# Kernel optimization log

Measured on AMD Instinct MI355X. Metric: run time of the kernel, lower is better.

The kernel has to match this reference:

```python
import jax, jax.numpy as jnp
from jax import lax
import numpy as np

N, C_IN, C_OUT, H, W_SP = 16, 16, 64, 256, 256
K, STRIDE, PAD = 3, 1, 1


def setup_inputs() -> dict:
    key = jax.random.key(0)
    k1, k2 = jax.random.split(key)
    x = jax.random.normal(k1, (N, C_IN, H, W_SP), dtype=jnp.float32)
    # One 3x3 filter per output channel (C_out independent Super0Net branches),
    # stacked into a single OIHW weight -> equivalent to the concatenated loop.
    W = jax.random.normal(k2, (C_OUT, C_IN, K, K), dtype=jnp.float32) * 0.05
    return {"x": x, "W": W}


def reference(x, W):
    # Fused form of: for ch in range(C_out): conv_ch(x) ; concat(dim=1).
    # Each branch is a Conv2d(C_in, 1, 3, stride=1, padding=1, bias=False).
    return lax.conv_general_dilated(
        x, W,
        window_strides=(STRIDE, STRIDE),
        padding=((PAD, PAD), (PAD, PAD)),
        dimension_numbers=("NCHW", "OIHW", "NCHW"),
    )
```

## Files before the change

### kernel.cpp

```cpp
#include <hip/hip_runtime.h>
#include <hip/hip_bf16.h>

typedef __attribute__((ext_vector_type(8))) __bf16 bf16x8;
typedef __attribute__((ext_vector_type(4))) float f32x4;

constexpr int CI_ = 16, CO_ = 64, H_ = 256, W_ = 256;
constexpr int WTROW = 168;
constexpr int RSZ = 258 * 32;

__device__ __forceinline__ unsigned swz(unsigned o) {
  return o ^ (((o >> 7) & 7u) << 4);
}

__global__ void transform_x_kernel(const float* __restrict__ x,
                                   unsigned short* __restrict__ xt) {
  int t = blockIdx.x * 256 + threadIdx.x;
  int p0 = t << 2;
  int w = p0 & 255;
  int h = (p0 >> 8) & 255;
  int n = p0 >> 16;
  const float* src = x + ((size_t)n * CI_) * (H_ * W_) + h * W_ + w;
  unsigned short tmp[64];
#pragma unroll
  for (int ci = 0; ci < 16; ++ci) {
    float4 v = *(const float4*)(src + (size_t)ci * (H_ * W_));
    tmp[0 * 16 + ci] = __builtin_bit_cast(unsigned short, (__bf16)v.x);
    tmp[1 * 16 + ci] = __builtin_bit_cast(unsigned short, (__bf16)v.y);
    tmp[2 * 16 + ci] = __builtin_bit_cast(unsigned short, (__bf16)v.z);
    tmp[3 * 16 + ci] = __builtin_bit_cast(unsigned short, (__bf16)v.w);
  }
  uint4* dst = (uint4*)(xt + (size_t)p0 * 16);
#pragma unroll
  for (int q = 0; q < 8; ++q) dst[q] = ((const uint4*)tmp)[q];
}

__global__ void transform_w_kernel(const float* __restrict__ Wg,
                                   unsigned short* __restrict__ wt) {
  int idx = blockIdx.x * 256 + threadIdx.x;
  int co = idx / WTROW;
  int kk = idx - co * WTROW;
  float v = 0.f;
  if (kk < 144) {
    int t = kk >> 4;
    int ci = kk & 15;
    v = Wg[(co * 16 + ci) * 9 + t];
  }
  wt[idx] = __builtin_bit_cast(unsigned short, (__bf16)v);
}

__global__ __launch_bounds__(256) void conv_mfma_kernel(
    const unsigned short* __restrict__ xt, const unsigned short* __restrict__ wt,
    float* __restrict__ out) {
  __shared__ unsigned char xs[3 * RSZ];
  __shared__ unsigned short wlds[CO_][WTROW];

  int tid = threadIdx.x;
  int bid = blockIdx.x;
  int h = bid & 255;
  int n = bid >> 8;

  {
    const uint4* src = (const uint4*)wt;
    uint4* dst = (uint4*)&wlds[0][0];
    for (int c = tid; c < 1344; c += 256) dst[c] = src[c];
  }
  {
    const uint4* srcbase = (const uint4*)xt;
    for (int c = tid; c < 1536; c += 256) {
      int r = c >> 9;
      int j = c & 511;
      int hh = h - 1 + r;
      uint4 v = make_uint4(0u, 0u, 0u, 0u);
      if (hh >= 0 && hh < 256)
        v = srcbase[(size_t)(n * 256 + hh) * 512 + j];
      *(uint4*)(xs + r * RSZ + swz(32u + 16u * (unsigned)j)) = v;
    }
    if (tid < 12) {
      int r = tid >> 2;
      int q = tid & 3;
      unsigned off = ((q >> 1) ? 257u * 32u : 0u) + (q & 1) * 16u;
      *(uint4*)(xs + r * RSZ + swz(off)) = make_uint4(0u, 0u, 0u, 0u);
    }
  }
  __syncthreads();

  int lane = tid & 63;
  int wave = tid >> 6;
  int col = lane & 15;
  int g = lane >> 4;

  f32x4 acc[4][4];
#pragma unroll
  for (int i = 0; i < 4; ++i)
#pragma unroll
    for (int j = 0; j < 4; ++j) acc[i][j] = (f32x4){0.f, 0.f, 0.f, 0.f};

  int pxb = wave * 64 + 4 * col;

#pragma unroll
  for (int s = 0; s < 5; ++s) {
    bf16x8 a[4];
#pragma unroll
    for (int cb = 0; cb < 4; ++cb)
      a[cb] = *(const bf16x8*)&wlds[cb * 16 + col][s * 32 + 8 * g];

    int tap = 2 * s + (g >> 1);
    if (tap > 8) tap = 8;
    int kh = tap / 3;
    int kw = tap - kh * 3;
    int ci0 = (g & 1) * 8;

    bf16x8 b[4];
#pragma unroll
    for (int pb = 0; pb < 4; ++pb) {
      unsigned wp = (unsigned)(pxb + pb + kw);
      b[pb] = *(const bf16x8*)(xs + kh * RSZ + swz(wp * 32u + ci0 * 2u));
    }

#pragma unroll
    for (int cb = 0; cb < 4; ++cb)
#pragma unroll
      for (int pb = 0; pb < 4; ++pb)
        acc[cb][pb] = __builtin_amdgcn_mfma_f32_16x16x32_bf16(
            a[cb], b[pb], acc[cb][pb], 0, 0, 0);
  }

  size_t obase = ((size_t)n * CO_ * H_ + h) * W_ + pxb;
#pragma unroll
  for (int cb = 0; cb < 4; ++cb) {
#pragma unroll
    for (int r = 0; r < 4; ++r) {
      int co = cb * 16 + g * 4 + r;
      f32x4 v = {acc[cb][0][r], acc[cb][1][r], acc[cb][2][r], acc[cb][3][r]};
      *(f32x4*)(out + obase + (size_t)co * (H_ * W_)) = v;
    }
  }
}

extern "C" void kernel_launch(void* const* d_in, const int* in_sizes, int n_in,
                              void* d_out, int out_size, void* d_ws, size_t ws_size,
                              hipStream_t stream) {
  const float* x = (const float*)d_in[0];
  const float* W = (const float*)d_in[1];
  float* out = (float*)d_out;

  unsigned short* xt = (unsigned short*)d_ws;
  unsigned short* wt = xt + (size_t)16 * 256 * 256 * 16;

  transform_x_kernel<<<1024, 256, 0, stream>>>(x, xt);
  transform_w_kernel<<<42, 256, 0, stream>>>(W, wt);
  conv_mfma_kernel<<<4096, 256, 0, stream>>>(xt, wt, out);
}
```

Baseline: 343.5 us.

## Fuse input NCHW-to-NHWC bf16 transform into conv kernel's LDS load

Removes the separate input transform kernel and its workspace round-trip. The conv kernel now reads fp32 NCHW rows directly, converts them to bf16 and writes channel-interleaved pairs into the swizzled LDS tile. The block index is also remapped so that neighbouring blocks land on different XCDs. The risk is redundant global reads, since each input row is fetched by three blocks in fp32, and narrower 4-byte LDS stores.

```diff
diff --git a/kernel.cpp b/kernel.cpp
--- a/kernel.cpp
+++ b/kernel.cpp
@@ -10,28 +10,6 @@
 
 __device__ __forceinline__ unsigned swz(unsigned o) {
   return o ^ (((o >> 7) & 7u) << 4);
-}
-
-__global__ void transform_x_kernel(const float* __restrict__ x,
-                                   unsigned short* __restrict__ xt) {
-  int t = blockIdx.x * 256 + threadIdx.x;
-  int p0 = t << 2;
-  int w = p0 & 255;
-  int h = (p0 >> 8) & 255;
-  int n = p0 >> 16;
-  const float* src = x + ((size_t)n * CI_) * (H_ * W_) + h * W_ + w;
-  unsigned short tmp[64];
-#pragma unroll
-  for (int ci = 0; ci < 16; ++ci) {
-    float4 v = *(const float4*)(src + (size_t)ci * (H_ * W_));
-    tmp[0 * 16 + ci] = __builtin_bit_cast(unsigned short, (__bf16)v.x);
-    tmp[1 * 16 + ci] = __builtin_bit_cast(unsigned short, (__bf16)v.y);
-    tmp[2 * 16 + ci] = __builtin_bit_cast(unsigned short, (__bf16)v.z);
-    tmp[3 * 16 + ci] = __builtin_bit_cast(unsigned short, (__bf16)v.w);
-  }
-  uint4* dst = (uint4*)(xt + (size_t)p0 * 16);
-#pragma unroll
-  for (int q = 0; q < 8; ++q) dst[q] = ((const uint4*)tmp)[q];
 }
 
 __global__ void transform_w_kernel(const float* __restrict__ Wg,
@@ -48,32 +26,52 @@
   wt[idx] = __builtin_bit_cast(unsigned short, (__bf16)v);
 }
 
-__global__ __launch_bounds__(256) void conv_mfma_kernel(
-    const unsigned short* __restrict__ xt, const unsigned short* __restrict__ wt,
+__global__ __launch_bounds__(256) void conv_fused_kernel(
+    const float* __restrict__ x, const unsigned short* __restrict__ wt,
     float* __restrict__ out) {
   __shared__ unsigned char xs[3 * RSZ];
   __shared__ unsigned short wlds[CO_][WTROW];
 
   int tid = threadIdx.x;
   int bid = blockIdx.x;
-  int h = bid & 255;
-  int n = bid >> 8;
+  int linear = (bid & 7) * 512 + (bid >> 3);
+  int h = linear & 255;
+  int n = linear >> 8;
+
+  int lane = tid & 63;
+  int wave = tid >> 6;
 
   {
     const uint4* src = (const uint4*)wt;
     uint4* dst = (uint4*)&wlds[0][0];
     for (int c = tid; c < 1344; c += 256) dst[c] = src[c];
   }
+
   {
-    const uint4* srcbase = (const uint4*)xt;
-    for (int c = tid; c < 1536; c += 256) {
-      int r = c >> 9;
-      int j = c & 511;
-      int hh = h - 1 + r;
-      uint4 v = make_uint4(0u, 0u, 0u, 0u);
-      if (hh >= 0 && hh < 256)
-        v = srcbase[(size_t)(n * 256 + hh) * 512 + j];
-      *(uint4*)(xs + r * RSZ + swz(32u + 16u * (unsigned)j)) = v;
+#pragma unroll
+    for (int u = 0; u < 6; ++u) {
+      int unit = wave * 6 + u;
+      int rr = unit >> 3;
+      int cp = unit & 7;
+      int hh = h - 1 + rr;
+      float4 va = make_float4(0.f, 0.f, 0.f, 0.f);
+      float4 vb = va;
+      if (hh >= 0 && hh < 256) {
+        const float* row =
+            x + (((size_t)(n * CI_ + 2 * cp)) * H_ + hh) * W_ + 4 * lane;
+        va = *(const float4*)row;
+        vb = *(const float4*)(row + H_ * W_);
+      }
+      float a4[4] = {va.x, va.y, va.z, va.w};
+      float b4[4] = {vb.x, vb.y, vb.z, vb.w};
+#pragma unroll
+      for (int k = 0; k < 4; ++k) {
+        unsigned wp = 4u * lane + 1u + k;
+        unsigned pa = __builtin_bit_cast(unsigned short, (__bf16)a4[k]);
+        unsigned pb = __builtin_bit_cast(unsigned short, (__bf16)b4[k]);
+        *(unsigned*)(xs + rr * RSZ + swz(wp * 32u + 4u * cp)) =
+            pa | (pb << 16);
+      }
     }
     if (tid < 12) {
       int r = tid >> 2;
@@ -84,8 +82,6 @@
   }
   __syncthreads();
 
-  int lane = tid & 63;
-  int wave = tid >> 6;
   int col = lane & 15;
   int g = lane >> 4;
 
@@ -144,10 +140,8 @@
   const float* W = (const float*)d_in[1];
   float* out = (float*)d_out;
 
-  unsigned short* xt = (unsigned short*)d_ws;
-  unsigned short* wt = xt + (size_t)16 * 256 * 256 * 16;
+  unsigned short* wt = (unsigned short*)d_ws;
 
-  transform_x_kernel<<<1024, 256, 0, stream>>>(x, xt);
   transform_w_kernel<<<42, 256, 0, stream>>>(W, wt);
-  conv_mfma_kernel<<<4096, 256, 0, stream>>>(xt, wt, out);
+  conv_fused_kernel<<<4096, 256, 0, stream>>>(x, wt, out);
 }
```

Result: slower. 352.4 us (+2.6%).
